# Optimization experiments

Hardware: AMD Instinct MI355X
Metric: run time of the kernel (lower is better)

Reference implementation:

```python
import jax, jax.numpy as jnp
import numpy as np

NUM_ITER = 3
NUM_SLOTS = 8
SLOT_SIZE = 128
MLP_HIDDEN = 256
EPSILON = 1e-8
INPUT_SIZE = 128
LN_EPS = 1e-5


def layer_norm(x):
    # parameter-free LayerNorm over last dim (LayerNorm() built with no args)
    mu = jnp.mean(x, axis=-1, keepdims=True)
    var = jnp.mean(jnp.square(x - mu), axis=-1, keepdims=True)
    return (x - mu) * jax.lax.rsqrt(var + LN_EPS)


def setup_inputs() -> dict:
    key = jax.random.key(0)
    ks = jax.random.split(key, 16)
    B, N, Din, D, H = 128, 4096, INPUT_SIZE, SLOT_SIZE, MLP_HIDDEN
    s_in = 1.0 / np.sqrt(Din)
    s_d = 1.0 / np.sqrt(D)
    s_h = 1.0 / np.sqrt(H)
    return {
        "inputs": jax.random.normal(ks[0], (B, N, Din), jnp.float32),
        "slots_noise": jax.random.normal(ks[1], (B, NUM_SLOTS, D), jnp.float32),
        "slots_mu": jax.random.normal(ks[2], (1, 1, D), jnp.float32),
        "slots_log_sigma": jax.random.normal(ks[3], (1, 1, D), jnp.float32) * 0.1,
        "Wq": jax.random.normal(ks[4], (D, D), jnp.float32) * s_d,
        "Wk": jax.random.normal(ks[5], (D, Din), jnp.float32) * s_in,
        "Wv": jax.random.normal(ks[6], (D, Din), jnp.float32) * s_in,
        "W_ih": jax.random.normal(ks[7], (3 * D, D), jnp.float32) * s_d,
        "W_hh": jax.random.normal(ks[8], (3 * D, D), jnp.float32) * s_d,
        "b_ih": jax.random.normal(ks[9], (3 * D,), jnp.float32) * s_d,
        "b_hh": jax.random.normal(ks[10], (3 * D,), jnp.float32) * s_d,
        "W1": jax.random.normal(ks[11], (H, D), jnp.float32) * s_d,
        "b1": jnp.zeros((H,), jnp.float32),
        "W2": jax.random.normal(ks[12], (D, H), jnp.float32) * s_h,
        "b2": jnp.zeros((D,), jnp.float32),
    }


def gru_cell(x, h, W_ih, W_hh, b_ih, b_hh):
    # PyTorch GRU, single step. x, h: (..., D)
    gx = x @ W_ih.T + b_ih  # (..., 3D)
    gh = h @ W_hh.T + b_hh
    D = h.shape[-1]
    xr, xz, xn = gx[..., :D], gx[..., D:2 * D], gx[..., 2 * D:]
    hr, hz, hn = gh[..., :D], gh[..., D:2 * D], gh[..., 2 * D:]
    r = jax.nn.sigmoid(xr + hr)
    z = jax.nn.sigmoid(xz + hz)
    n = jnp.tanh(xn + r * hn)
    return (1.0 - z) * n + z * h


def reference(inputs, slots_noise, slots_mu, slots_log_sigma, Wq, Wk, Wv,
              W_ih, W_hh, b_ih, b_hh, W1, b1, W2, b2):
    scale = 1.0 / np.sqrt(SLOT_SIZE)
    x = layer_norm(inputs)                      # (B, N, Din)
    k = x @ Wk.T                                # (B, N, D)
    v = x @ Wv.T                                # (B, N, D)
    slots = slots_mu + jnp.exp(slots_log_sigma) * slots_noise  # (B, S, D)
    for _ in range(NUM_ITER):
        slots_n = layer_norm(slots)             # NOTE: GRU hidden is the NORMED slots (matches source)
        q = slots_n @ Wq.T                      # (B, S, D)
        logits = jnp.einsum("bnd,bsd->bns", k, q) * scale  # (B, N, S)
        attn = jax.nn.softmax(logits, axis=-1) + EPSILON
        attn = attn / jnp.sum(attn, axis=-2, keepdims=True)
        updates = jnp.einsum("bns,bnd->bsd", attn, v)      # (B, S, D)
        slots = gru_cell(updates, slots_n, W_ih, W_hh, b_ih, b_hh)
        slots = slots + (jax.nn.relu(layer_norm(slots) @ W1.T + b1) @ W2.T + b2)
    return slots
```

## Files before the change

kernel.cpp:

```cpp
#include <hip/hip_runtime.h>
#include <math.h>


typedef __attribute__((ext_vector_type(4))) float fx4;
typedef __attribute__((ext_vector_type(8))) short sx8;
typedef __attribute__((ext_vector_type(8))) __bf16 bfx8;
typedef __attribute__((ext_vector_type(4))) unsigned short ux4;

static __device__ __forceinline__ fx4 MFMA(sx8 a, sx8 b, fx4 c) {
  return __builtin_amdgcn_mfma_f32_16x16x32_bf16(
      __builtin_bit_cast(bfx8, a), __builtin_bit_cast(bfx8, b), c, 0, 0, 0);
}

static __device__ __forceinline__ unsigned short f2bf(float f) {
  union { float f; unsigned u; } x; x.f = f;
  unsigned r = x.u + 0x7fffu + ((x.u >> 16) & 1u);
  return (unsigned short)(r >> 16);
}
static __device__ __forceinline__ float bf2f(unsigned short u) {
  union { unsigned u; float f; } x; x.u = ((unsigned)u) << 16; return x.f;
}
static __device__ __forceinline__ fx4 ntload4(const float* p) {
  return __builtin_nontemporal_load((const fx4*)p);
}

__global__ __launch_bounds__(256) void k_fold(
    const float* __restrict__ Wq, const float* __restrict__ Wk,
    const float* __restrict__ Wih, const float* __restrict__ Wv,
    float* __restrict__ Wqk, float* __restrict__ Wihv) {
  int idx = blockIdx.x * 256 + threadIdx.x;
  if (idx < 16384) {
    int e = idx >> 7, c = idx & 127;
    float s = 0.f;
#pragma unroll 4
    for (int d = 0; d < 128; d++) s += Wq[d * 128 + e] * Wk[d * 128 + c];
    Wqk[idx] = s * 0.08838834764831845f;
    return;
  }
  idx -= 16384;
  if (idx < 49152) {
    int g = idx >> 7, c = idx & 127;
    float s = 0.f;
#pragma unroll 4
    for (int d = 0; d < 128; d++) s += Wih[g * 128 + d] * Wv[d * 128 + c];
    Wihv[idx] = s;
  }
}

__global__ __launch_bounds__(256) void k_pack(
    const float* __restrict__ noise, const float* __restrict__ mu,
    const float* __restrict__ lsig, const float* __restrict__ Wqk,
    const float* __restrict__ Wihv, const float* __restrict__ Whh,
    const float* __restrict__ W1, const float* __restrict__ W2,
    float* __restrict__ slots, unsigned short* __restrict__ wqk_b,
    unsigned short* __restrict__ wihv_b, unsigned short* __restrict__ whh_b,
    unsigned short* __restrict__ w1_b, unsigned short* __restrict__ w2_b) {
  int idx = blockIdx.x * 256 + threadIdx.x;
  if (idx < 131072) {
    int d = idx & 127;
    slots[idx] = mu[d] + expf(lsig[d]) * noise[idx];
    return;
  }
  idx -= 131072;
  if (idx < 16384) {
    wqk_b[idx] = f2bf(Wqk[(idx & 127) * 128 + (idx >> 7)]);
    return;
  }
  idx -= 16384;
  if (idx < 49152) { wihv_b[idx] = f2bf(Wihv[idx]); return; }
  idx -= 49152;
  if (idx < 49152) { whh_b[idx] = f2bf(Whh[idx]); return; }
  idx -= 49152;
  if (idx < 32768) { w1_b[idx] = f2bf(W1[idx]); return; }
  idx -= 32768;
  w2_b[idx] = f2bf(W2[idx]);
}

__global__ __launch_bounds__(64) void k_slot_pre(
    const float* __restrict__ slots, const unsigned short* __restrict__ wqk_b,
    float* __restrict__ slots_n, unsigned short* __restrict__ q2_b) {
  __shared__ __align__(16) short xf[4 * 64 * 8];
  int l = threadIdx.x;
  int r = l & 15, seg = l >> 4;
  long rowbase = (long)blockIdx.x * 16;
  {
    const float* xp = slots + (rowbase + r) * 128 + seg * 32;
    float* snp = slots_n + (rowbase + r) * 128 + seg * 32;
    float v[32];
    float s = 0.f, s2 = 0.f;
#pragma unroll
    for (int i = 0; i < 8; i++) {
      fx4 t = *(const fx4*)(xp + i * 4);
      v[i * 4 + 0] = t.x; v[i * 4 + 1] = t.y; v[i * 4 + 2] = t.z; v[i * 4 + 3] = t.w;
      s += t.x + t.y + t.z + t.w;
      s2 += t.x * t.x + t.y * t.y + t.z * t.z + t.w * t.w;
    }
    s += __shfl_xor(s, 16, 64);  s += __shfl_xor(s, 32, 64);
    s2 += __shfl_xor(s2, 16, 64); s2 += __shfl_xor(s2, 32, 64);
    float mean = s * 0.0078125f;
    float var = s2 * 0.0078125f - mean * mean;
    float rstd = rsqrtf(var + 1e-5f);
#pragma unroll
    for (int i = 0; i < 8; i++) {
      fx4 t = {(v[i * 4 + 0] - mean) * rstd, (v[i * 4 + 1] - mean) * rstd,
               (v[i * 4 + 2] - mean) * rstd, (v[i * 4 + 3] - mean) * rstd};
      *(fx4*)(snp + i * 4) = t;
      v[i * 4 + 0] = t.x; v[i * 4 + 1] = t.y; v[i * 4 + 2] = t.z; v[i * 4 + 3] = t.w;
    }
#pragma unroll
    for (int q = 0; q < 4; q++) {
      sx8 t;
#pragma unroll
      for (int j = 0; j < 8; j++) t[j] = (short)f2bf(v[q * 8 + j]);
      *(sx8*)&xf[(seg * 64 + (r + 16 * q)) * 8] = t;
    }
  }
  __syncthreads();
  const fx4 z4 = {0.f, 0.f, 0.f, 0.f};
  fx4 acc[8];
#pragma unroll
  for (int nt = 0; nt < 8; nt++) acc[nt] = z4;
#pragma unroll
  for (int ks = 0; ks < 4; ks++) {
    sx8 a = *(const sx8*)&xf[(ks * 64 + l) * 8];
#pragma unroll
    for (int nt = 0; nt < 8; nt++) {
      sx8 bfr = *(const sx8*)(wqk_b + (nt * 16 + (l & 15)) * 128 + ks * 32 + (l >> 4) * 8);
      acc[nt] = MFMA(a, bfr, acc[nt]);
    }
  }
  int cl = l & 15, rq = (l >> 4) * 4;
#pragma unroll
  for (int nt = 0; nt < 8; nt++)
#pragma unroll
    for (int rg = 0; rg < 4; rg++)
      q2_b[(rowbase + rq + rg) * 128 + nt * 16 + cl] = f2bf(acc[nt][rg]);
}

__global__ __launch_bounds__(256) void k_attn(
    const unsigned short* __restrict__ ln16, const unsigned short* __restrict__ q2b,
    float* __restrict__ upd_part, float* __restrict__ sattn_part) {
  __shared__ __align__(16) float abuf[4 * 1024];
  __shared__ float sattnbuf[4 * 8];
  int tid = threadIdx.x, w = tid >> 6, l = tid & 63;
  int b = blockIdx.x >> 4, c = blockIdx.x & 15;
  long base = (long)b * 4096 + (c * 4 + w) * 64;
  const unsigned short* xt = ln16 + base * 128;
  int s = l & 15, qd = (l >> 4) * 8;
  sx8 qf[4];
#pragma unroll
  for (int ks = 0; ks < 4; ks++) {
    if (s < 8) {
      qf[ks] = *(const sx8*)(q2b + ((long)b * 8 + s) * 128 + ks * 32 + qd);
    } else {
      sx8 t;
#pragma unroll
      for (int j = 0; j < 8; j++) t[j] = 0;
      qf[ks] = t;
    }
  }
  sx8 a[4][4];
#pragma unroll
  for (int mt = 0; mt < 4; mt++)
#pragma unroll
    for (int ks = 0; ks < 4; ks++)
      a[mt][ks] = *(const sx8*)(xt + (mt * 16 + s) * 128 + ks * 32 + qd);
  const fx4 z4 = {0.f, 0.f, 0.f, 0.f};
  float sat_loc = 0.f;
  float ua[4][4] = {};
  int d0 = (l & 31) * 4, s0 = (l >> 5) * 4;
  float* attnw = abuf + w * 1024;
#pragma unroll
  for (int mt = 0; mt < 4; mt++) {
    fx4 cc = z4;
#pragma unroll
    for (int ks = 0; ks < 4; ks++) cc = MFMA(a[mt][ks], qf[ks], cc);
#pragma unroll
    for (int rg = 0; rg < 4; rg++) {
      float lg = cc[rg];
      float mx = lg;
      mx = fmaxf(mx, __shfl_xor(mx, 1, 64));
      mx = fmaxf(mx, __shfl_xor(mx, 2, 64));
      mx = fmaxf(mx, __shfl_xor(mx, 4, 64));
      float p = __expf(lg - mx);
      float sm = p;
      sm += __shfl_xor(sm, 1, 64);
      sm += __shfl_xor(sm, 2, 64);
      sm += __shfl_xor(sm, 4, 64);
      float at = p / sm + 1e-8f;
      if (s < 8) sat_loc += at;
      attnw[(mt * 16 + (l >> 4) * 4 + rg) * 16 + s] = at;
    }
  }
#pragma unroll 2
  for (int n0 = 0; n0 < 64; n0 += 8) {
    ux4 vv[8]; fx4 at4[8];
#pragma unroll
    for (int u = 0; u < 8; u++) {
      vv[u] = *(const ux4*)(xt + (n0 + u) * 128 + d0);
      at4[u] = *(const fx4*)&attnw[(n0 + u) * 16 + s0];
    }
#pragma unroll
    for (int u = 0; u < 8; u++) {
      float v0 = bf2f(vv[u].x), v1 = bf2f(vv[u].y), v2 = bf2f(vv[u].z), v3 = bf2f(vv[u].w);
#pragma unroll
      for (int si = 0; si < 4; si++) {
        float av = at4[u][si];
        ua[si][0] += av * v0; ua[si][1] += av * v1;
        ua[si][2] += av * v2; ua[si][3] += av * v3;
      }
    }
  }
#pragma unroll
  for (int si = 0; si < 4; si++) {
    fx4 tv = {ua[si][0], ua[si][1], ua[si][2], ua[si][3]};
    *(fx4*)&attnw[(s0 + si) * 128 + d0] = tv;
  }
  sat_loc += __shfl_xor(sat_loc, 16, 64);
  sat_loc += __shfl_xor(sat_loc, 32, 64);
  if (l < 8) sattnbuf[w * 8 + l] = sat_loc;
  __syncthreads();
  {
    int i = tid * 4;
    fx4 o = *(const fx4*)&abuf[i] + *(const fx4*)&abuf[1024 + i] +
            *(const fx4*)&abuf[2048 + i] + *(const fx4*)&abuf[3072 + i];
    *(fx4*)(upd_part + ((size_t)(b * 16 + c)) * 1024 + i) = o;
    if (tid < 8)
      sattn_part[(b * 16 + c) * 8 + tid] =
          sattnbuf[tid] + sattnbuf[8 + tid] + sattnbuf[16 + tid] + sattnbuf[24 + tid];
  }
}

__global__ __launch_bounds__(256) void k_attn_first(
    const float* __restrict__ x, unsigned short* __restrict__ ln16,
    const unsigned short* __restrict__ q2b,
    float* __restrict__ upd_part, float* __restrict__ sattn_part) {
  __shared__ __align__(16) float abuf[4 * 1024];
  __shared__ float sattnbuf[4 * 8];
  int tid = threadIdx.x, w = tid >> 6, l = tid & 63;
  int b = blockIdx.x >> 4, c = blockIdx.x & 15;
  long base = (long)b * 4096 + (c * 4 + w) * 64;
  const float* xs = x + base * 128;
  unsigned short* xt = ln16 + base * 128;
  int s = l & 15, qd = (l >> 4) * 8;
  sx8 qf[4];
#pragma unroll
  for (int ks = 0; ks < 4; ks++) {
    if (s < 8) {
      qf[ks] = *(const sx8*)(q2b + ((long)b * 8 + s) * 128 + ks * 32 + qd);
    } else {
      sx8 t;
#pragma unroll
      for (int j = 0; j < 8; j++) t[j] = 0;
      qf[ks] = t;
    }
  }
  sx8 a[4][4];
#pragma unroll
  for (int mt = 0; mt < 4; mt++) {
    const float* rp = xs + (mt * 16 + s) * 128 + qd;
    float v[32];
    float sm = 0.f, s2 = 0.f;
#pragma unroll
    for (int ks = 0; ks < 4; ks++) {
      fx4 t0 = ntload4(rp + ks * 32);
      fx4 t1 = ntload4(rp + ks * 32 + 4);
      v[ks * 8 + 0] = t0.x; v[ks * 8 + 1] = t0.y; v[ks * 8 + 2] = t0.z; v[ks * 8 + 3] = t0.w;
      v[ks * 8 + 4] = t1.x; v[ks * 8 + 5] = t1.y; v[ks * 8 + 6] = t1.z; v[ks * 8 + 7] = t1.w;
      sm += t0.x + t0.y + t0.z + t0.w + t1.x + t1.y + t1.z + t1.w;
      s2 += t0.x * t0.x + t0.y * t0.y + t0.z * t0.z + t0.w * t0.w +
            t1.x * t1.x + t1.y * t1.y + t1.z * t1.z + t1.w * t1.w;
    }
    sm += __shfl_xor(sm, 16, 64);  sm += __shfl_xor(sm, 32, 64);
    s2 += __shfl_xor(s2, 16, 64);  s2 += __shfl_xor(s2, 32, 64);
    float mean = sm * 0.0078125f;
    float rstd = rsqrtf(s2 * 0.0078125f - mean * mean + 1e-5f);
#pragma unroll
    for (int ks = 0; ks < 4; ks++) {
      sx8 t;
#pragma unroll
      for (int j = 0; j < 8; j++) t[j] = (short)f2bf((v[ks * 8 + j] - mean) * rstd);
      a[mt][ks] = t;
      *(sx8*)(xt + (mt * 16 + s) * 128 + ks * 32 + qd) = t;
    }
  }
  __threadfence_block();
  const fx4 z4 = {0.f, 0.f, 0.f, 0.f};
  float sat_loc = 0.f;
  float ua[4][4] = {};
  int d0 = (l & 31) * 4, s0 = (l >> 5) * 4;
  float* attnw = abuf + w * 1024;
#pragma unroll
  for (int mt = 0; mt < 4; mt++) {
    fx4 cc = z4;
#pragma unroll
    for (int ks = 0; ks < 4; ks++) cc = MFMA(a[mt][ks], qf[ks], cc);
#pragma unroll
    for (int rg = 0; rg < 4; rg++) {
      float lg = cc[rg];
      float mx = lg;
      mx = fmaxf(mx, __shfl_xor(mx, 1, 64));
      mx = fmaxf(mx, __shfl_xor(mx, 2, 64));
      mx = fmaxf(mx, __shfl_xor(mx, 4, 64));
      float p = __expf(lg - mx);
      float sm = p;
      sm += __shfl_xor(sm, 1, 64);
      sm += __shfl_xor(sm, 2, 64);
      sm += __shfl_xor(sm, 4, 64);
      float at = p / sm + 1e-8f;
      if (s < 8) sat_loc += at;
      attnw[(mt * 16 + (l >> 4) * 4 + rg) * 16 + s] = at;
    }
  }
#pragma unroll 2
  for (int n0 = 0; n0 < 64; n0 += 8) {
    ux4 vv[8]; fx4 at4[8];
#pragma unroll
    for (int u = 0; u < 8; u++) {
      vv[u] = *(const ux4*)(xt + (n0 + u) * 128 + d0);
      at4[u] = *(const fx4*)&attnw[(n0 + u) * 16 + s0];
    }
#pragma unroll
    for (int u = 0; u < 8; u++) {
      float v0 = bf2f(vv[u].x), v1 = bf2f(vv[u].y), v2 = bf2f(vv[u].z), v3 = bf2f(vv[u].w);
#pragma unroll
      for (int si = 0; si < 4; si++) {
        float av = at4[u][si];
        ua[si][0] += av * v0; ua[si][1] += av * v1;
        ua[si][2] += av * v2; ua[si][3] += av * v3;
      }
    }
  }
#pragma unroll
  for (int si = 0; si < 4; si++) {
    fx4 tv = {ua[si][0], ua[si][1], ua[si][2], ua[si][3]};
    *(fx4*)&attnw[(s0 + si) * 128 + d0] = tv;
  }
  sat_loc += __shfl_xor(sat_loc, 16, 64);
  sat_loc += __shfl_xor(sat_loc, 32, 64);
  if (l < 8) sattnbuf[w * 8 + l] = sat_loc;
  __syncthreads();
  {
    int i = tid * 4;
    fx4 o = *(const fx4*)&abuf[i] + *(const fx4*)&abuf[1024 + i] +
            *(const fx4*)&abuf[2048 + i] + *(const fx4*)&abuf[3072 + i];
    *(fx4*)(upd_part + ((size_t)(b * 16 + c)) * 1024 + i) = o;
    if (tid < 8)
      sattn_part[(b * 16 + c) * 8 + tid] =
          sattnbuf[tid] + sattnbuf[8 + tid] + sattnbuf[16 + tid] + sattnbuf[24 + tid];
  }
}

__global__ __launch_bounds__(256) void k_slot_post(
    const float* __restrict__ upd_part, const float* __restrict__ sattn_part,
    float* __restrict__ slots_n,
    const unsigned short* __restrict__ wihv_b, const unsigned short* __restrict__ whh_b,
    const float* __restrict__ b_ih, const float* __restrict__ b_hh,
    const unsigned short* __restrict__ w1_b, const float* __restrict__ b1,
    const unsigned short* __restrict__ w2_b, const float* __restrict__ b2,
    const unsigned short* __restrict__ wqk_b,
    unsigned short* __restrict__ q2_b, float* __restrict__ out_final, int final_flag) {
  __shared__ __align__(16) char smem[78336];
  float* gx = (float*)smem;
  float* gh = (float*)(smem + 24576);
  float* xred = gx;
  short* xfr = (short*)(smem + 49152);
  short* hfr = (short*)(smem + 53248);
  short* ynf = (short*)(smem + 57344);
  short* y1f = (short*)(smem + 61440);
  float* snew = (float*)(smem + 69632);
  float* satred = (float*)(smem + 78080);
  int tid = threadIdx.x, w = tid >> 6, l = tid & 63;
  int rowbase = blockIdx.x * 16;
  int r = l & 15, seg = l >> 4;
  {
    int row = rowbase + r;
    int bb = row >> 3, ss = row & 7;
    float a[32];
#pragma unroll
    for (int i = 0; i < 32; i++) a[i] = 0.f;
    float satsum = 0.f;
#pragma unroll
    for (int ci = 0; ci < 4; ci++) {
      int ch = bb * 16 + w * 4 + ci;
      const float* up = upd_part + (size_t)ch * 1024 + ss * 128 + seg * 32;
#pragma unroll
      for (int i = 0; i < 8; i++) {
        fx4 t = *(const fx4*)(up + i * 4);
        a[i * 4 + 0] += t.x; a[i * 4 + 1] += t.y; a[i * 4 + 2] += t.z; a[i * 4 + 3] += t.w;
      }
      satsum += sattn_part[ch * 8 + ss];
    }
#pragma unroll
    for (int i = 0; i < 8; i++) {
      fx4 t = {a[i * 4], a[i * 4 + 1], a[i * 4 + 2], a[i * 4 + 3]};
      *(fx4*)&xred[w * 2048 + r * 128 + seg * 32 + i * 4] = t;
    }
    if (seg == 0) satred[w * 16 + r] = satsum;
  }
  __syncthreads();
  if (w == 0) {
    float inv = 1.f / (satred[r] + satred[16 + r] + satred[32 + r] + satred[48 + r]);
    float a[32];
#pragma unroll
    for (int i = 0; i < 8; i++) {
      fx4 t = *(const fx4*)&xred[r * 128 + seg * 32 + i * 4];
      fx4 t1 = *(const fx4*)&xred[2048 + r * 128 + seg * 32 + i * 4];
      fx4 t2 = *(const fx4*)&xred[4096 + r * 128 + seg * 32 + i * 4];
      fx4 t3 = *(const fx4*)&xred[6144 + r * 128 + seg * 32 + i * 4];
      t = t + t1 + t2 + t3;
      a[i * 4 + 0] = t.x * inv; a[i * 4 + 1] = t.y * inv;
      a[i * 4 + 2] = t.z * inv; a[i * 4 + 3] = t.w * inv;
    }
#pragma unroll
    for (int q = 0; q < 4; q++) {
      sx8 t;
#pragma unroll
      for (int j = 0; j < 8; j++) t[j] = (short)f2bf(a[q * 8 + j]);
      *(sx8*)&xfr[(seg * 64 + (r + 16 * q)) * 8] = t;
    }
  } else if (w == 1) {
    const float* hp = slots_n + (long)(rowbase + r) * 128 + seg * 32;
#pragma unroll
    for (int q = 0; q < 4; q++) {
      fx4 t0 = *(const fx4*)(hp + q * 8);
      fx4 t1 = *(const fx4*)(hp + q * 8 + 4);
      sx8 t;
      t[0] = (short)f2bf(t0.x); t[1] = (short)f2bf(t0.y);
      t[2] = (short)f2bf(t0.z); t[3] = (short)f2bf(t0.w);
      t[4] = (short)f2bf(t1.x); t[5] = (short)f2bf(t1.y);
      t[6] = (short)f2bf(t1.z); t[7] = (short)f2bf(t1.w);
      *(sx8*)&hfr[(seg * 64 + (r + 16 * q)) * 8] = t;
    }
  }
  __syncthreads();
  const fx4 z4 = {0.f, 0.f, 0.f, 0.f};
  {
    fx4 ax[6], ah[6];
#pragma unroll
    for (int j = 0; j < 6; j++) { ax[j] = z4; ah[j] = z4; }
#pragma unroll
    for (int ks = 0; ks < 4; ks++) {
      sx8 a_x = *(const sx8*)&xfr[(ks * 64 + l) * 8];
      sx8 a_h = *(const sx8*)&hfr[(ks * 64 + l) * 8];
#pragma unroll
      for (int j = 0; j < 6; j++) {
        int nt = w * 6 + j;
        sx8 bx = *(const sx8*)(wihv_b + (nt * 16 + (l & 15)) * 128 + ks * 32 + (l >> 4) * 8);
        sx8 bh = *(const sx8*)(whh_b + (nt * 16 + (l & 15)) * 128 + ks * 32 + (l >> 4) * 8);
        ax[j] = MFMA(a_x, bx, ax[j]);
        ah[j] = MFMA(a_h, bh, ah[j]);
      }
    }
#pragma unroll
    for (int j = 0; j < 6; j++) {
      int col = (w * 6 + j) * 16 + (l & 15);
#pragma unroll
      for (int rg = 0; rg < 4; rg++) {
        int row = (l >> 4) * 4 + rg;
        gx[row * 384 + col] = ax[j][rg];
        gh[row * 384 + col] = ah[j][rg];
      }
    }
  }
  __syncthreads();
  {
    int row = tid >> 4, j0 = (tid & 15) * 8;
#pragma unroll
    for (int j = j0; j < j0 + 8; j++) {
      float xr = gx[row * 384 + j] + b_ih[j];
      float xz = gx[row * 384 + 128 + j] + b_ih[128 + j];
      float xn = gx[row * 384 + 256 + j] + b_ih[256 + j];
      float hr = gh[row * 384 + j] + b_hh[j];
      float hz = gh[row * 384 + 128 + j] + b_hh[128 + j];
      float hn = gh[row * 384 + 256 + j] + b_hh[256 + j];
      float rr = 1.f / (1.f + __expf(-(xr + hr)));
      float zz = 1.f / (1.f + __expf(-(xz + hz)));
      float nn = tanhf(xn + rr * hn);
      float h = slots_n[(long)(rowbase + row) * 128 + j];
      snew[row * 132 + j] = (1.f - zz) * nn + zz * h;
    }
  }
  __syncthreads();
  if (w == 0) {
    float v[32];
    float s = 0.f, s2 = 0.f;
#pragma unroll
    for (int i = 0; i < 32; i++) {
      float t = snew[r * 132 + seg * 32 + i];
      v[i] = t; s += t; s2 += t * t;
    }
    s += __shfl_xor(s, 16, 64);  s += __shfl_xor(s, 32, 64);
    s2 += __shfl_xor(s2, 16, 64); s2 += __shfl_xor(s2, 32, 64);
    float mean = s * 0.0078125f;
    float var = s2 * 0.0078125f - mean * mean;
    float rstd = rsqrtf(var + 1e-5f);
#pragma unroll
    for (int q = 0; q < 4; q++) {
      sx8 t;
#pragma unroll
      for (int j = 0; j < 8; j++) t[j] = (short)f2bf((v[q * 8 + j] - mean) * rstd);
      *(sx8*)&ynf[(seg * 64 + (r + 16 * q)) * 8] = t;
    }
  }
  __syncthreads();
  {
    fx4 y[4];
#pragma unroll
    for (int j = 0; j < 4; j++) y[j] = z4;
#pragma unroll
    for (int ks = 0; ks < 4; ks++) {
      sx8 a = *(const sx8*)&ynf[(ks * 64 + l) * 8];
#pragma unroll
      for (int j = 0; j < 4; j++) {
        int nt = w * 4 + j;
        sx8 bf = *(const sx8*)(w1_b + (nt * 16 + (l & 15)) * 128 + ks * 32 + (l >> 4) * 8);
        y[j] = MFMA(a, bf, y[j]);
      }
    }
#pragma unroll
    for (int j = 0; j < 4; j++) {
      int col = (w * 4 + j) * 16 + (l & 15);
      float bias = b1[col];
      int ks3 = col >> 5, qq = (col >> 3) & 3, jj = col & 7;
#pragma unroll
      for (int rg = 0; rg < 4; rg++) {
        float val = fmaxf(y[j][rg] + bias, 0.f);
        int m = (l >> 4) * 4 + rg;
        y1f[(ks3 * 64 + m + 16 * qq) * 8 + jj] = (short)f2bf(val);
      }
    }
  }
  __syncthreads();
  {
    fx4 zz2[2];
    zz2[0] = z4; zz2[1] = z4;
#pragma unroll
    for (int ks = 0; ks < 8; ks++) {
      sx8 a = *(const sx8*)&y1f[(ks * 64 + l) * 8];
#pragma unroll
      for (int j = 0; j < 2; j++) {
        sx8 bf = *(const sx8*)(w2_b + ((w * 2 + j) * 16 + (l & 15)) * 256 + ks * 32 + (l >> 4) * 8);
        zz2[j] = MFMA(a, bf, zz2[j]);
      }
    }
#pragma unroll
    for (int j = 0; j < 2; j++) {
      int col = (w * 2 + j) * 16 + (l & 15);
      float bias = b2[col];
#pragma unroll
      for (int rg = 0; rg < 4; rg++) {
        int row = (l >> 4) * 4 + rg;
        snew[row * 132 + col] += zz2[j][rg] + bias;
      }
    }
  }
  __syncthreads();
  if (final_flag) {
    int row = tid >> 4, c8 = (tid & 15) * 8;
    fx4 t0 = *(const fx4*)&snew[row * 132 + c8];
    fx4 t1 = *(const fx4*)&snew[row * 132 + c8 + 4];
    *(fx4*)(out_final + (long)(rowbase + row) * 128 + c8) = t0;
    *(fx4*)(out_final + (long)(rowbase + row) * 128 + c8 + 4) = t1;
    return;
  }
  if (w == 0) {
    float v[32];
    float s = 0.f, s2 = 0.f;
#pragma unroll
    for (int i = 0; i < 32; i++) {
      float t = snew[r * 132 + seg * 32 + i];
      v[i] = t; s += t; s2 += t * t;
    }
    s += __shfl_xor(s, 16, 64);  s += __shfl_xor(s, 32, 64);
    s2 += __shfl_xor(s2, 16, 64); s2 += __shfl_xor(s2, 32, 64);
    float mean = s * 0.0078125f;
    float var = s2 * 0.0078125f - mean * mean;
    float rstd = rsqrtf(var + 1e-5f);
    float* snp = slots_n + (long)(rowbase + r) * 128 + seg * 32;
#pragma unroll
    for (int i = 0; i < 8; i++) {
      fx4 t = {(v[i * 4 + 0] - mean) * rstd, (v[i * 4 + 1] - mean) * rstd,
               (v[i * 4 + 2] - mean) * rstd, (v[i * 4 + 3] - mean) * rstd};
      *(fx4*)(snp + i * 4) = t;
      v[i * 4 + 0] = t.x; v[i * 4 + 1] = t.y; v[i * 4 + 2] = t.z; v[i * 4 + 3] = t.w;
    }
#pragma unroll
    for (int q = 0; q < 4; q++) {
      sx8 t;
#pragma unroll
      for (int j = 0; j < 8; j++) t[j] = (short)f2bf(v[q * 8 + j]);
      *(sx8*)&ynf[(seg * 64 + (r + 16 * q)) * 8] = t;
    }
  }
  __syncthreads();
  {
    fx4 acc2[2];
    acc2[0] = z4; acc2[1] = z4;
#pragma unroll
    for (int ks = 0; ks < 4; ks++) {
      sx8 a = *(const sx8*)&ynf[(ks * 64 + l) * 8];
#pragma unroll
      for (int j = 0; j < 2; j++) {
        int nt = w * 2 + j;
        sx8 bf = *(const sx8*)(wqk_b + (nt * 16 + (l & 15)) * 128 + ks * 32 + (l >> 4) * 8);
        acc2[j] = MFMA(a, bf, acc2[j]);
      }
    }
    int cl = l & 15, rq = (l >> 4) * 4;
#pragma unroll
    for (int j = 0; j < 2; j++) {
      int nt = w * 2 + j;
#pragma unroll
      for (int rg = 0; rg < 4; rg++)
        q2_b[(long)(rowbase + rq + rg) * 128 + nt * 16 + cl] = f2bf(acc2[j][rg]);
    }
  }
}

extern "C" void kernel_launch(void* const* d_in, const int* in_sizes, int n_in,
                              void* d_out, int out_size, void* d_ws, size_t ws_size,
                              hipStream_t stream) {
  (void)in_sizes; (void)n_in; (void)out_size; (void)ws_size;
  const float* x = (const float*)d_in[0];
  const float* noise = (const float*)d_in[1];
  const float* mu = (const float*)d_in[2];
  const float* lsig = (const float*)d_in[3];
  const float* Wq = (const float*)d_in[4];
  const float* Wk = (const float*)d_in[5];
  const float* Wv = (const float*)d_in[6];
  const float* Wih = (const float*)d_in[7];
  const float* Whh = (const float*)d_in[8];
  const float* b_ih = (const float*)d_in[9];
  const float* b_hh = (const float*)d_in[10];
  const float* W1 = (const float*)d_in[11];
  const float* b1 = (const float*)d_in[12];
  const float* W2 = (const float*)d_in[13];
  const float* b2 = (const float*)d_in[14];

  char* ws = (char*)d_ws;
  size_t off = 0;
  auto take = [&](size_t bytes) {
    char* p = ws + off;
    off += (bytes + 255) & ~(size_t)255;
    return p;
  };
  unsigned short* ln16 = (unsigned short*)take(134217728);
  float* Wqk = (float*)take(65536);
  float* Wihv = (float*)take(196608);
  unsigned short* wqk_b = (unsigned short*)take(32768);
  unsigned short* wihv_b = (unsigned short*)take(98304);
  unsigned short* whh_b = (unsigned short*)take(98304);
  unsigned short* w1_b = (unsigned short*)take(65536);
  unsigned short* w2_b = (unsigned short*)take(65536);
  float* slots = (float*)take(524288);
  float* slots_n = (float*)take(524288);
  unsigned short* q2_b = (unsigned short*)take(262144);
  float* upd_part = (float*)take(8388608);
  float* sattn_part = (float*)take(65536);

  k_fold<<<256, 256, 0, stream>>>(Wq, Wk, Wih, Wv, Wqk, Wihv);
  k_pack<<<1216, 256, 0, stream>>>(noise, mu, lsig, Wqk, Wihv, Whh, W1, W2,
                                   slots, wqk_b, wihv_b, whh_b, w1_b, w2_b);
  k_slot_pre<<<64, 64, 0, stream>>>(slots, wqk_b, slots_n, q2_b);
  k_attn_first<<<2048, 256, 0, stream>>>(x, ln16, q2_b, upd_part, sattn_part);
  k_slot_post<<<64, 256, 0, stream>>>(upd_part, sattn_part, slots_n, wihv_b, whh_b,
                                      b_ih, b_hh, w1_b, b1, w2_b, b2, wqk_b,
                                      q2_b, (float*)d_out, 0);
  for (int it = 1; it < 3; it++) {
    k_attn<<<2048, 256, 0, stream>>>(ln16, q2_b, upd_part, sattn_part);
    k_slot_post<<<64, 256, 0, stream>>>(upd_part, sattn_part, slots_n, wihv_b, whh_b,
                                        b_ih, b_hh, w1_b, b1, w2_b, b2, wqk_b,
                                        q2_b, (float*)d_out, (it == 2) ? 1 : 0);
  }
}
```

Baseline: 602.8 us.

## Compute attention-weighted value sum with split-bf16 MFMA instead of scalar FMAs

The attn·V accumulation in both attention kernels moves from scalar fp32 FMAs over LDS-staged fp32 attention weights onto 16x16x32 bf16 MFMAs. Attention weights are split into high and low bf16 parts, staged in a padded LDS buffer, and multiplied against V fragments gathered with strided 2-byte global loads. This aims to cut VALU work, at the cost of doubled MFMAs for precision and uncoalesced per-element V loads that may hurt memory efficiency.

```diff
diff --git a/kernel.cpp b/kernel.cpp
--- a/kernel.cpp
+++ b/kernel.cpp
@@ -4,6 +4,7 @@
 
 typedef __attribute__((ext_vector_type(4))) float fx4;
 typedef __attribute__((ext_vector_type(8))) short sx8;
+typedef __attribute__((ext_vector_type(4))) short sx4;
 typedef __attribute__((ext_vector_type(8))) __bf16 bfx8;
 typedef __attribute__((ext_vector_type(4))) unsigned short ux4;
 
@@ -23,6 +24,8 @@
 static __device__ __forceinline__ fx4 ntload4(const float* p) {
   return __builtin_nontemporal_load((const fx4*)p);
 }
+
+#define PSTR 72
 
 __global__ __launch_bounds__(256) void k_fold(
     const float* __restrict__ Wq, const float* __restrict__ Wk,
@@ -141,12 +144,13 @@
     const unsigned short* __restrict__ ln16, const unsigned short* __restrict__ q2b,
     float* __restrict__ upd_part, float* __restrict__ sattn_part) {
   __shared__ __align__(16) float abuf[4 * 1024];
+  __shared__ __align__(16) short plds[4][2][16 * PSTR];
   __shared__ float sattnbuf[4 * 8];
   int tid = threadIdx.x, w = tid >> 6, l = tid & 63;
   int b = blockIdx.x >> 4, c = blockIdx.x & 15;
   long base = (long)b * 4096 + (c * 4 + w) * 64;
   const unsigned short* xt = ln16 + base * 128;
-  int s = l & 15, qd = (l >> 4) * 8;
+  int s = l & 15, seg = l >> 4, qd = seg * 8;
   sx8 qf[4];
 #pragma unroll
   for (int ks = 0; ks < 4; ks++) {
@@ -159,22 +163,19 @@
       qf[ks] = t;
     }
   }
-  sx8 a[4][4];
-#pragma unroll
-  for (int mt = 0; mt < 4; mt++)
-#pragma unroll
-    for (int ks = 0; ks < 4; ks++)
-      a[mt][ks] = *(const sx8*)(xt + (mt * 16 + s) * 128 + ks * 32 + qd);
   const fx4 z4 = {0.f, 0.f, 0.f, 0.f};
   float sat_loc = 0.f;
-  float ua[4][4] = {};
-  int d0 = (l & 31) * 4, s0 = (l >> 5) * 4;
-  float* attnw = abuf + w * 1024;
+  short* ph = &plds[w][0][0];
+  short* pl = &plds[w][1][0];
 #pragma unroll
   for (int mt = 0; mt < 4; mt++) {
     fx4 cc = z4;
 #pragma unroll
-    for (int ks = 0; ks < 4; ks++) cc = MFMA(a[mt][ks], qf[ks], cc);
+    for (int ks = 0; ks < 4; ks++) {
+      sx8 a = *(const sx8*)(xt + (mt * 16 + s) * 128 + ks * 32 + qd);
+      cc = MFMA(a, qf[ks], cc);
+    }
+    sx4 hv, lv;
 #pragma unroll
     for (int rg = 0; rg < 4; rg++) {
       float lg = cc[rg];
@@ -189,32 +190,36 @@
       sm += __shfl_xor(sm, 4, 64);
       float at = p / sm + 1e-8f;
       if (s < 8) sat_loc += at;
-      attnw[(mt * 16 + (l >> 4) * 4 + rg) * 16 + s] = at;
-    }
-  }
-#pragma unroll 2
-  for (int n0 = 0; n0 < 64; n0 += 8) {
-    ux4 vv[8]; fx4 at4[8];
-#pragma unroll
-    for (int u = 0; u < 8; u++) {
-      vv[u] = *(const ux4*)(xt + (n0 + u) * 128 + d0);
-      at4[u] = *(const fx4*)&attnw[(n0 + u) * 16 + s0];
-    }
-#pragma unroll
-    for (int u = 0; u < 8; u++) {
-      float v0 = bf2f(vv[u].x), v1 = bf2f(vv[u].y), v2 = bf2f(vv[u].z), v3 = bf2f(vv[u].w);
-#pragma unroll
-      for (int si = 0; si < 4; si++) {
-        float av = at4[u][si];
-        ua[si][0] += av * v0; ua[si][1] += av * v1;
-        ua[si][2] += av * v2; ua[si][3] += av * v3;
-      }
-    }
-  }
-#pragma unroll
-  for (int si = 0; si < 4; si++) {
-    fx4 tv = {ua[si][0], ua[si][1], ua[si][2], ua[si][3]};
-    *(fx4*)&attnw[(s0 + si) * 128 + d0] = tv;
+      unsigned short hb = f2bf(at);
+      hv[rg] = (short)hb;
+      lv[rg] = (short)f2bf(at - bf2f(hb));
+    }
+    *(sx4*)&ph[s * PSTR + mt * 16 + seg * 4] = hv;
+    *(sx4*)&pl[s * PSTR + mt * 16 + seg * 4] = lv;
+  }
+  fx4 acc[8];
+#pragma unroll
+  for (int nt = 0; nt < 8; nt++) acc[nt] = z4;
+#pragma unroll
+  for (int ks2 = 0; ks2 < 2; ks2++) {
+    sx8 pah = *(const sx8*)&ph[s * PSTR + ks2 * 32 + seg * 8];
+    sx8 pal = *(const sx8*)&pl[s * PSTR + ks2 * 32 + seg * 8];
+#pragma unroll
+    for (int nt = 0; nt < 8; nt++) {
+      const unsigned short* cp = xt + (ks2 * 32 + seg * 8) * 128 + nt * 16 + s;
+      sx8 bfr;
+#pragma unroll
+      for (int j = 0; j < 8; j++) bfr[j] = (short)cp[j * 128];
+      acc[nt] = MFMA(pah, bfr, acc[nt]);
+      acc[nt] = MFMA(pal, bfr, acc[nt]);
+    }
+  }
+  if (seg < 2) {
+#pragma unroll
+    for (int nt = 0; nt < 8; nt++)
+#pragma unroll
+      for (int rg = 0; rg < 4; rg++)
+        abuf[w * 1024 + (seg * 4 + rg) * 128 + nt * 16 + s] = acc[nt][rg];
   }
   sat_loc += __shfl_xor(sat_loc, 16, 64);
   sat_loc += __shfl_xor(sat_loc, 32, 64);
@@ -236,13 +241,14 @@
     const unsigned short* __restrict__ q2b,
     float* __restrict__ upd_part, float* __restrict__ sattn_part) {
   __shared__ __align__(16) float abuf[4 * 1024];
+  __shared__ __align__(16) short plds[4][2][16 * PSTR];
   __shared__ float sattnbuf[4 * 8];
   int tid = threadIdx.x, w = tid >> 6, l = tid & 63;
   int b = blockIdx.x >> 4, c = blockIdx.x & 15;
   long base = (long)b * 4096 + (c * 4 + w) * 64;
   const float* xs = x + base * 128;
   unsigned short* xt = ln16 + base * 128;
-  int s = l & 15, qd = (l >> 4) * 8;
+  int s = l & 15, seg = l >> 4, qd = seg * 8;
   sx8 qf[4];
 #pragma unroll
   for (int ks = 0; ks < 4; ks++) {
@@ -255,7 +261,10 @@
       qf[ks] = t;
     }
   }
-  sx8 a[4][4];
+  const fx4 z4 = {0.f, 0.f, 0.f, 0.f};
+  float sat_loc = 0.f;
+  short* ph = &plds[w][0][0];
+  short* pl = &plds[w][1][0];
 #pragma unroll
   for (int mt = 0; mt < 4; mt++) {
     const float* rp = xs + (mt * 16 + s) * 128 + qd;
@@ -275,26 +284,16 @@
     s2 += __shfl_xor(s2, 16, 64);  s2 += __shfl_xor(s2, 32, 64);
     float mean = sm * 0.0078125f;
     float rstd = rsqrtf(s2 * 0.0078125f - mean * mean + 1e-5f);
+    fx4 cc = z4;
 #pragma unroll
     for (int ks = 0; ks < 4; ks++) {
       sx8 t;
 #pragma unroll
       for (int j = 0; j < 8; j++) t[j] = (short)f2bf((v[ks * 8 + j] - mean) * rstd);
-      a[mt][ks] = t;
       *(sx8*)(xt + (mt * 16 + s) * 128 + ks * 32 + qd) = t;
-    }
-  }
-  __threadfence_block();
-  const fx4 z4 = {0.f, 0.f, 0.f, 0.f};
-  float sat_loc = 0.f;
-  float ua[4][4] = {};
-  int d0 = (l & 31) * 4, s0 = (l >> 5) * 4;
-  float* attnw = abuf + w * 1024;
-#pragma unroll
-  for (int mt = 0; mt < 4; mt++) {
-    fx4 cc = z4;
-#pragma unroll
-    for (int ks = 0; ks < 4; ks++) cc = MFMA(a[mt][ks], qf[ks], cc);
+      cc = MFMA(t, qf[ks], cc);
+    }
+    sx4 hv, lv;
 #pragma unroll
     for (int rg = 0; rg < 4; rg++) {
       float lg = cc[rg];
@@ -303,38 +302,43 @@
       mx = fmaxf(mx, __shfl_xor(mx, 2, 64));
       mx = fmaxf(mx, __shfl_xor(mx, 4, 64));
       float p = __expf(lg - mx);
-      float sm = p;
-      sm += __shfl_xor(sm, 1, 64);
-      sm += __shfl_xor(sm, 2, 64);
-      sm += __shfl_xor(sm, 4, 64);
-      float at = p / sm + 1e-8f;
+      float smm = p;
+      smm += __shfl_xor(smm, 1, 64);
+      smm += __shfl_xor(smm, 2, 64);
+      smm += __shfl_xor(smm, 4, 64);
+      float at = p / smm + 1e-8f;
       if (s < 8) sat_loc += at;
-      attnw[(mt * 16 + (l >> 4) * 4 + rg) * 16 + s] = at;
-    }
-  }
-#pragma unroll 2
-  for (int n0 = 0; n0 < 64; n0 += 8) {
-    ux4 vv[8]; fx4 at4[8];
-#pragma unroll
-    for (int u = 0; u < 8; u++) {
-      vv[u] = *(const ux4*)(xt + (n0 + u) * 128 + d0);
-      at4[u] = *(const fx4*)&attnw[(n0 + u) * 16 + s0];
-    }
-#pragma unroll
-    for (int u = 0; u < 8; u++) {
-      float v0 = bf2f(vv[u].x), v1 = bf2f(vv[u].y), v2 = bf2f(vv[u].z), v3 = bf2f(vv[u].w);
-#pragma unroll
-      for (int si = 0; si < 4; si++) {
-        float av = at4[u][si];
-        ua[si][0] += av * v0; ua[si][1] += av * v1;
-        ua[si][2] += av * v2; ua[si][3] += av * v3;
-      }
-    }
-  }
-#pragma unroll
-  for (int si = 0; si < 4; si++) {
-    fx4 tv = {ua[si][0], ua[si][1], ua[si][2], ua[si][3]};
-    *(fx4*)&attnw[(s0 + si) * 128 + d0] = tv;
+      unsigned short hb = f2bf(at);
+      hv[rg] = (short)hb;
+      lv[rg] = (short)f2bf(at - bf2f(hb));
+    }
+    *(sx4*)&ph[s * PSTR + mt * 16 + seg * 4] = hv;
+    *(sx4*)&pl[s * PSTR + mt * 16 + seg * 4] = lv;
+  }
+  __threadfence_block();
+  fx4 acc[8];
+#pragma unroll
+  for (int nt = 0; nt < 8; nt++) acc[nt] = z4;
+#pragma unroll
+  for (int ks2 = 0; ks2 < 2; ks2++) {
+    sx8 pah = *(const sx8*)&ph[s * PSTR + ks2 * 32 + seg * 8];
+    sx8 pal = *(const sx8*)&pl[s * PSTR + ks2 * 32 + seg * 8];
+#pragma unroll
+    for (int nt = 0; nt < 8; nt++) {
+      const unsigned short* cp = xt + (ks2 * 32 + seg * 8) * 128 + nt * 16 + s;
+      sx8 bfr;
+#pragma unroll
+      for (int j = 0; j < 8; j++) bfr[j] = (short)cp[j * 128];
+      acc[nt] = MFMA(pah, bfr, acc[nt]);
+      acc[nt] = MFMA(pal, bfr, acc[nt]);
+    }
+  }
+  if (seg < 2) {
+#pragma unroll
+    for (int nt = 0; nt < 8; nt++)
+#pragma unroll
+      for (int rg = 0; rg < 4; rg++)
+        abuf[w * 1024 + (seg * 4 + rg) * 128 + nt * 16 + s] = acc[nt][rg];
   }
   sat_loc += __shfl_xor(sat_loc, 16, 64);
   sat_loc += __shfl_xor(sat_loc, 32, 64);
```

Result: faster. 584.9 us (-3.0%).
